# Kernel tuning notes

Measured on AMD Instinct MI355X. Metric: run time of the kernel, lower is better.

The kernel has to match this reference:

```python
import jax, jax.numpy as jnp
import numpy as np

B, T, D, H, C = 128, 1024, 3, 512, 3


def setup_inputs() -> dict:
    key = jax.random.key(0)
    ks = jax.random.split(key, 9)
    s = 1.0 / np.sqrt(H)
    u = lambda k, shp: jax.random.uniform(k, shp, jnp.float32, -s, s)
    return {
        'inputs': jax.random.normal(ks[0], (B, T, D), jnp.float32),
        'W': u(ks[1], (H, H)),
        'P': u(ks[2], (H, D)),
        'b_v': u(ks[3], (H, 1)),
        'W_z': u(ks[4], (H, H)),
        'P_z': u(ks[5], (H, D)),
        'b_z': u(ks[6], (H, 1)),
        'fc_W': u(ks[7], (C, H)),
        'fc_b': u(ks[8], (C,)),
    }


def reference(inputs, W, P, b_v, W_z, P_z, b_z, fc_W, fc_b):
    # Mask: second half of hidden units receive no direct input (rows H//2: of P zeroed)
    h = P.shape[0]
    P_m = jnp.concatenate([P[: h // 2], jnp.zeros_like(P[h // 2 :])], axis=0)
    bv = b_v[:, 0]
    bz = b_z[:, 0]

    def step(r, x_t):  # r: (B,H), x_t: (B,D)
        z = jax.nn.sigmoid(r @ W_z.T + x_t @ P_z.T + bz)
        cand = jax.nn.sigmoid(r @ W.T + x_t @ P_m.T + bv)
        r_new = (1.0 - z) * r + z * cand
        return r_new, r_new

    r0 = jnp.zeros((inputs.shape[0], h), inputs.dtype)
    xs = jnp.transpose(inputs, (1, 0, 2))  # (T,B,D)
    _, hs = jax.lax.scan(step, r0, xs)      # (T,B,H)
    hidden = jnp.transpose(hs, (1, 0, 2))   # (B,T,H)
    out = hidden @ fc_W.T + fc_b            # (B,T,C)
    return out, hidden
```

## Files before the change

### kernel.cpp

```cpp
#include <hip/hip_runtime.h>
#include <hip/hip_bf16.h>

#define BB 128
#define TT 1024
#define DD 3
#define HH 512
#define CC 3

#define NG 8
#define NCH 16
#define MB 16
#define HC 32

typedef __attribute__((ext_vector_type(8))) __bf16 bf16x8;
typedef __attribute__((ext_vector_type(4))) float f32x4;

__global__ __launch_bounds__(256, 1) void rnn_persist(
    const float* __restrict__ x,
    const float* __restrict__ W,
    const float* __restrict__ P,
    const float* __restrict__ bv,
    const float* __restrict__ Wz,
    const float* __restrict__ Pz,
    const float* __restrict__ bz,
    float* __restrict__ hidden,
    unsigned* __restrict__ Rbuf,
    unsigned* __restrict__ ready)
{
    __shared__ __align__(16) __bf16 Wl[64][520];
    __shared__ __align__(16) __bf16 Ra[16][520];
    __shared__ float pre[16][68];

    const int tid = threadIdx.x;
    const int bid = blockIdx.x;
    const int g   = bid & 7;
    const int ch  = bid >> 3;
    const int h0  = ch * HC;
    const int b0  = g * MB;

    for (int idx = tid; idx < 64 * 512; idx += 256) {
        int row = idx >> 9, col = idx & 511;
        float v = (row < 32) ? Wz[(h0 + row) * HH + col]
                             : W[(h0 + row - 32) * HH + col];
        Wl[row][col] = (__bf16)v;
    }

    const int lane = tid & 63;
    const int wv   = tid >> 6;
    const int frow = lane & 15;
    const int q    = lane >> 4;
    const int eb   = tid >> 4;
    const int ehp  = tid & 15;

    const int hl0 = 2 * ehp, hl1 = hl0 + 1;
    const int hg0 = h0 + hl0, hg1 = h0 + hl1;
    const float pzw00 = Pz[hg0*3+0], pzw01 = Pz[hg0*3+1], pzw02 = Pz[hg0*3+2];
    const float pzw10 = Pz[hg1*3+0], pzw11 = Pz[hg1*3+1], pzw12 = Pz[hg1*3+2];
    const float pvw00 = (hg0 < HH/2) ? P[hg0*3+0] : 0.f;
    const float pvw01 = (hg0 < HH/2) ? P[hg0*3+1] : 0.f;
    const float pvw02 = (hg0 < HH/2) ? P[hg0*3+2] : 0.f;
    const float pvw10 = (hg1 < HH/2) ? P[hg1*3+0] : 0.f;
    const float pvw11 = (hg1 < HH/2) ? P[hg1*3+1] : 0.f;
    const float pvw12 = (hg1 < HH/2) ? P[hg1*3+2] : 0.f;
    const float bzr0 = bz[hg0], bzr1 = bz[hg1];
    const float bvr0 = bv[hg0], bvr1 = bv[hg1];

    {
        uint2 cl; cl.x = 0xFFFFFFFFu; cl.y = 0xFFFFFFFFu;
        unsigned* d0 = Rbuf + (size_t)(b0 + eb) * HH + h0 + hl0;
        unsigned* d1 = d0 + BB * HH;
        asm volatile("global_store_dwordx2 %0, %2, off sc0 sc1\n\t"
                     "global_store_dwordx2 %1, %2, off sc0 sc1\n\t"
                     "s_waitcnt vmcnt(0)"
                     :: "v"(d0), "v"(d1), "v"(cl) : "memory");
    }
    __syncthreads();
    if (tid == 0)
        __hip_atomic_store(&ready[bid], 1u, __ATOMIC_RELAXED, __HIP_MEMORY_SCOPE_AGENT);
    if (tid < 16) {
        const unsigned* rp = &ready[tid * 8 + g];
        int spin = 0;
        while (__hip_atomic_load(rp, __ATOMIC_RELAXED, __HIP_MEMORY_SCOPE_AGENT) == 0u) {
            if (++spin > (1 << 20)) break;
        }
    }
    __syncthreads();

    bf16x8 Bfrag[16];
    #pragma unroll
    for (int ks = 0; ks < 16; ks++)
        Bfrag[ks] = *(const bf16x8*)&Wl[wv * 16 + frow][ks * 32 + q * 8];

    float rs0 = 0.f, rs1 = 0.f;
    const float* xptr = x + (size_t)(b0 + eb) * TT * DD;

    const int c4 = tid & 127;
    const int r0 = tid >> 7;
    char* rb = (char*)&Ra[0][0] + r0 * 1040 + c4 * 8;

    #define BAD4(G) ((((G).x ^ w16) | ((G).y ^ w16) | ((G).z ^ w16) | ((G).w ^ w16)) & 0xFFFFu)

    for (int t = 0; t < TT; t++) {
        float x0 = xptr[0], x1 = xptr[1], x2 = xptr[2];
        xptr += DD;

        float mz0, mz1, mc0, mc1;
        if (t > 0) {
            const unsigned w16 = (unsigned)t;
            const unsigned* bse = Rbuf + (size_t)(t & 1) * (BB * HH)
                                + (size_t)(b0 + r0) * HH + (c4 << 2);
            const uint4* q0 = (const uint4*)(bse);
            const uint4* q1 = (const uint4*)(bse + 1024);
            const uint4* q2 = (const uint4*)(bse + 2048);
            const uint4* q3 = (const uint4*)(bse + 3072);
            const uint4* q4 = (const uint4*)(bse + 4096);
            const uint4* q5 = (const uint4*)(bse + 5120);
            const uint4* q6 = (const uint4*)(bse + 6144);
            const uint4* q7 = (const uint4*)(bse + 7168);
            uint4 G0, G1, G2, G3, G4, G5, G6, G7;
            int spin = 0;
            for (;;) {
                asm volatile(
                    "global_load_dwordx4 %0, %8, off sc0 sc1\n\t"
                    "global_load_dwordx4 %1, %9, off sc0 sc1\n\t"
                    "global_load_dwordx4 %2, %10, off sc0 sc1\n\t"
                    "global_load_dwordx4 %3, %11, off sc0 sc1\n\t"
                    "global_load_dwordx4 %4, %12, off sc0 sc1\n\t"
                    "global_load_dwordx4 %5, %13, off sc0 sc1\n\t"
                    "global_load_dwordx4 %6, %14, off sc0 sc1\n\t"
                    "global_load_dwordx4 %7, %15, off sc0 sc1\n\t"
                    "s_waitcnt vmcnt(0)"
                    : "=&v"(G0), "=&v"(G1), "=&v"(G2), "=&v"(G3),
                      "=&v"(G4), "=&v"(G5), "=&v"(G6), "=&v"(G7)
                    : "v"(q0), "v"(q1), "v"(q2), "v"(q3),
                      "v"(q4), "v"(q5), "v"(q6), "v"(q7)
                    : "memory");
                unsigned bad = BAD4(G0) | BAD4(G1) | BAD4(G2) | BAD4(G3)
                             | BAD4(G4) | BAD4(G5) | BAD4(G6) | BAD4(G7);
                if (bad == 0u) break;
                if (++spin > (1 << 12)) break;
            }
            { uint2 o; o.x=(G0.x>>16)|(G0.y&0xFFFF0000u); o.y=(G0.z>>16)|(G0.w&0xFFFF0000u);
              *(uint2*)(rb + 0*2080) = o; }
            { uint2 o; o.x=(G1.x>>16)|(G1.y&0xFFFF0000u); o.y=(G1.z>>16)|(G1.w&0xFFFF0000u);
              *(uint2*)(rb + 1*2080) = o; }
            { uint2 o; o.x=(G2.x>>16)|(G2.y&0xFFFF0000u); o.y=(G2.z>>16)|(G2.w&0xFFFF0000u);
              *(uint2*)(rb + 2*2080) = o; }
            { uint2 o; o.x=(G3.x>>16)|(G3.y&0xFFFF0000u); o.y=(G3.z>>16)|(G3.w&0xFFFF0000u);
              *(uint2*)(rb + 3*2080) = o; }
            { uint2 o; o.x=(G4.x>>16)|(G4.y&0xFFFF0000u); o.y=(G4.z>>16)|(G4.w&0xFFFF0000u);
              *(uint2*)(rb + 4*2080) = o; }
            { uint2 o; o.x=(G5.x>>16)|(G5.y&0xFFFF0000u); o.y=(G5.z>>16)|(G5.w&0xFFFF0000u);
              *(uint2*)(rb + 5*2080) = o; }
            { uint2 o; o.x=(G6.x>>16)|(G6.y&0xFFFF0000u); o.y=(G6.z>>16)|(G6.w&0xFFFF0000u);
              *(uint2*)(rb + 6*2080) = o; }
            { uint2 o; o.x=(G7.x>>16)|(G7.y&0xFFFF0000u); o.y=(G7.z>>16)|(G7.w&0xFFFF0000u);
              *(uint2*)(rb + 7*2080) = o; }
            __syncthreads();

            f32x4 acc = {0.f, 0.f, 0.f, 0.f};
            #pragma unroll
            for (int ks = 0; ks < 16; ks++) {
                bf16x8 af = *(const bf16x8*)&Ra[frow][ks * 32 + q * 8];
                acc = __builtin_amdgcn_mfma_f32_16x16x32_bf16(af, Bfrag[ks], acc, 0, 0, 0);
            }
            #pragma unroll
            for (int r = 0; r < 4; r++)
                pre[q * 4 + r][wv * 16 + frow] = acc[r];
            __syncthreads();

            mz0 = pre[eb][hl0];      mz1 = pre[eb][hl1];
            mc0 = pre[eb][32 + hl0]; mc1 = pre[eb][32 + hl1];
        } else {
            mz0 = mz1 = mc0 = mc1 = 0.f;
        }

        float pz0 = mz0 + x0*pzw00 + x1*pzw01 + x2*pzw02 + bzr0;
        float pz1 = mz1 + x0*pzw10 + x1*pzw11 + x2*pzw12 + bzr1;
        float pv0 = mc0 + x0*pvw00 + x1*pvw01 + x2*pvw02 + bvr0;
        float pv1 = mc1 + x0*pvw10 + x1*pvw11 + x2*pvw12 + bvr1;
        float z0 = 1.f / (1.f + __expf(-pz0));
        float z1 = 1.f / (1.f + __expf(-pz1));
        float c0 = 1.f / (1.f + __expf(-pv0));
        float c1 = 1.f / (1.f + __expf(-pv1));
        rs0 = (1.f - z0) * rs0 + z0 * c0;
        rs1 = (1.f - z1) * rs1 + z1 * c1;

        if (t < TT - 1) {
            unsigned tagv = (unsigned)(t + 1);
            union { __bf16 h; unsigned short u; } a0, a1;
            a0.h = (__bf16)rs0; a1.h = (__bf16)rs1;
            uint2 d; d.x = ((unsigned)a0.u << 16) | tagv;
                     d.y = ((unsigned)a1.u << 16) | tagv;
            unsigned* dst = Rbuf + (size_t)((t + 1) & 1) * (BB * HH)
                          + (size_t)(b0 + eb) * HH + h0 + hl0;
            asm volatile("global_store_dwordx2 %0, %1, off sc0 sc1"
                         :: "v"(dst), "v"(d) : "memory");
        }
        union { float f[2]; uint2 u2; } hvu;
        hvu.f[0] = rs0; hvu.f[1] = rs1;
        float* hid = &hidden[((size_t)(b0 + eb) * TT + t) * HH + h0 + hl0];
        asm volatile("global_store_dwordx2 %0, %1, off"
                     :: "v"(hid), "v"(hvu.u2) : "memory");
    }
    #undef BAD4
}

__global__ __launch_bounds__(256) void fc_kernel(
    const float* __restrict__ hidden, const float* __restrict__ fcW,
    const float* __restrict__ fcb, float* __restrict__ out)
{
    const int lane = threadIdx.x & 63;
    const int wid  = (blockIdx.x * blockDim.x + threadIdx.x) >> 6;
    const int nw   = (gridDim.x * blockDim.x) >> 6;
    const int NR   = BB * TT;

    float w0[8], w1[8], w2[8];
    #pragma unroll
    for (int j = 0; j < 8; j++) {
        w0[j] = fcW[0 * HH + lane * 8 + j];
        w1[j] = fcW[1 * HH + lane * 8 + j];
        w2[j] = fcW[2 * HH + lane * 8 + j];
    }
    const float c0 = fcb[0], c1 = fcb[1], c2 = fcb[2];

    int row = wid;
    float4 va, vb;
    if (row < NR) {
        const float* hr = hidden + (size_t)row * HH + lane * 8;
        va = *(const float4*)hr;
        vb = *(const float4*)(hr + 4);
    }
    while (row < NR) {
        int nrow = row + nw;
        float4 na, nb;
        if (nrow < NR) {
            const float* hr = hidden + (size_t)nrow * HH + lane * 8;
            na = *(const float4*)hr;
            nb = *(const float4*)(hr + 4);
        }
        float s0 = va.x*w0[0] + va.y*w0[1] + va.z*w0[2] + va.w*w0[3]
                 + vb.x*w0[4] + vb.y*w0[5] + vb.z*w0[6] + vb.w*w0[7];
        float s1 = va.x*w1[0] + va.y*w1[1] + va.z*w1[2] + va.w*w1[3]
                 + vb.x*w1[4] + vb.y*w1[5] + vb.z*w1[6] + vb.w*w1[7];
        float s2 = va.x*w2[0] + va.y*w2[1] + va.z*w2[2] + va.w*w2[3]
                 + vb.x*w2[4] + vb.y*w2[5] + vb.z*w2[6] + vb.w*w2[7];
        #pragma unroll
        for (int off = 1; off < 64; off <<= 1) {
            s0 += __shfl_xor(s0, off);
            s1 += __shfl_xor(s1, off);
            s2 += __shfl_xor(s2, off);
        }
        if (lane == 0) {
            float* o = out + (size_t)row * CC;
            o[0] = s0 + c0; o[1] = s1 + c1; o[2] = s2 + c2;
        }
        row = nrow; va = na; vb = nb;
    }
}

extern "C" void kernel_launch(void* const* d_in, const int* in_sizes, int n_in,
                              void* d_out, int out_size, void* d_ws, size_t ws_size,
                              hipStream_t stream) {
    (void)in_sizes; (void)n_in; (void)out_size; (void)ws_size;
    const float* x   = (const float*)d_in[0];
    const float* W   = (const float*)d_in[1];
    const float* P   = (const float*)d_in[2];
    const float* bv  = (const float*)d_in[3];
    const float* Wz  = (const float*)d_in[4];
    const float* Pz  = (const float*)d_in[5];
    const float* bz  = (const float*)d_in[6];
    const float* fcW = (const float*)d_in[7];
    const float* fcb = (const float*)d_in[8];

    float* out    = (float*)d_out;
    float* hidden = out + (size_t)BB * TT * CC;

    unsigned* ready = (unsigned*)d_ws;
    unsigned* Rbuf  = (unsigned*)((char*)d_ws + 4096);

    hipMemsetAsync(d_ws, 0, 4096, stream);
    hipLaunchKernelGGL(rnn_persist, dim3(NG * NCH), dim3(256), 0, stream,
                       x, W, P, bv, Wz, Pz, bz, hidden, Rbuf, ready);
    hipLaunchKernelGGL(fc_kernel, dim3(1024), dim3(256), 0, stream,
                       hidden, fcW, fcb, out);
}
```

Measured before the change: 2.421 ms.

## Halve persistent blocks, widen hidden slice per block, add cheap tag pre-poll

Cuts the persistent RNN grid from 128 to 64 blocks, so each block owns 64 hidden units and runs two MFMA accumulators per wave against twice the LDS-resident weights. Each thread now handles four hidden units and writes 128-bit stores. Before the full-tile load, one wave polls a single tag word from each producer block and only then issues the bulk load. The aim is to reduce per-step cross-block synchronisation traffic and polling contention, at the cost of doubling per-block MFMA and elementwise work on the serial critical path.

```diff
diff --git a/kernel.cpp b/kernel.cpp
--- a/kernel.cpp
+++ b/kernel.cpp
@@ -8,12 +8,13 @@
 #define CC 3
 
 #define NG 8
-#define NCH 16
+#define NCH 8
 #define MB 16
-#define HC 32
+#define HC 64
 
 typedef __attribute__((ext_vector_type(8))) __bf16 bf16x8;
 typedef __attribute__((ext_vector_type(4))) float f32x4;
+typedef __attribute__((ext_vector_type(4))) unsigned u32x4;
 
 __global__ __launch_bounds__(256, 1) void rnn_persist(
     const float* __restrict__ x,
@@ -27,9 +28,9 @@
     unsigned* __restrict__ Rbuf,
     unsigned* __restrict__ ready)
 {
-    __shared__ __align__(16) __bf16 Wl[64][520];
+    __shared__ __align__(16) __bf16 Wl[128][520];
     __shared__ __align__(16) __bf16 Ra[16][520];
-    __shared__ float pre[16][68];
+    __shared__ float pre[16][132];
 
     const int tid = threadIdx.x;
     const int bid = blockIdx.x;
@@ -38,10 +39,10 @@
     const int h0  = ch * HC;
     const int b0  = g * MB;
 
-    for (int idx = tid; idx < 64 * 512; idx += 256) {
+    for (int idx = tid; idx < 128 * 512; idx += 256) {
         int row = idx >> 9, col = idx & 511;
-        float v = (row < 32) ? Wz[(h0 + row) * HH + col]
-                             : W[(h0 + row - 32) * HH + col];
+        float v = (row < 64) ? Wz[(h0 + row) * HH + col]
+                             : W[(h0 + row - 64) * HH + col];
         Wl[row][col] = (__bf16)v;
     }
 
@@ -50,48 +51,58 @@
     const int frow = lane & 15;
     const int q    = lane >> 4;
     const int eb   = tid >> 4;
-    const int ehp  = tid & 15;
-
-    const int hl0 = 2 * ehp, hl1 = hl0 + 1;
-    const int hg0 = h0 + hl0, hg1 = h0 + hl1;
-    const float pzw00 = Pz[hg0*3+0], pzw01 = Pz[hg0*3+1], pzw02 = Pz[hg0*3+2];
-    const float pzw10 = Pz[hg1*3+0], pzw11 = Pz[hg1*3+1], pzw12 = Pz[hg1*3+2];
-    const float pvw00 = (hg0 < HH/2) ? P[hg0*3+0] : 0.f;
-    const float pvw01 = (hg0 < HH/2) ? P[hg0*3+1] : 0.f;
-    const float pvw02 = (hg0 < HH/2) ? P[hg0*3+2] : 0.f;
-    const float pvw10 = (hg1 < HH/2) ? P[hg1*3+0] : 0.f;
-    const float pvw11 = (hg1 < HH/2) ? P[hg1*3+1] : 0.f;
-    const float pvw12 = (hg1 < HH/2) ? P[hg1*3+2] : 0.f;
-    const float bzr0 = bz[hg0], bzr1 = bz[hg1];
-    const float bvr0 = bv[hg0], bvr1 = bv[hg1];
+    const int ehq  = tid & 15;
+    const int hl   = ehq * 4;
+
+    const int hg0 = h0 + hl, hg1 = hg0 + 1, hg2 = hg0 + 2, hg3 = hg0 + 3;
+    const float pz00 = Pz[hg0*3+0], pz01 = Pz[hg0*3+1], pz02 = Pz[hg0*3+2];
+    const float pz10 = Pz[hg1*3+0], pz11 = Pz[hg1*3+1], pz12 = Pz[hg1*3+2];
+    const float pz20 = Pz[hg2*3+0], pz21 = Pz[hg2*3+1], pz22 = Pz[hg2*3+2];
+    const float pz30 = Pz[hg3*3+0], pz31 = Pz[hg3*3+1], pz32 = Pz[hg3*3+2];
+    const float pv00 = (hg0 < HH/2) ? P[hg0*3+0] : 0.f;
+    const float pv01 = (hg0 < HH/2) ? P[hg0*3+1] : 0.f;
+    const float pv02 = (hg0 < HH/2) ? P[hg0*3+2] : 0.f;
+    const float pv10 = (hg1 < HH/2) ? P[hg1*3+0] : 0.f;
+    const float pv11 = (hg1 < HH/2) ? P[hg1*3+1] : 0.f;
+    const float pv12 = (hg1 < HH/2) ? P[hg1*3+2] : 0.f;
+    const float pv20 = (hg2 < HH/2) ? P[hg2*3+0] : 0.f;
+    const float pv21 = (hg2 < HH/2) ? P[hg2*3+1] : 0.f;
+    const float pv22 = (hg2 < HH/2) ? P[hg2*3+2] : 0.f;
+    const float pv30 = (hg3 < HH/2) ? P[hg3*3+0] : 0.f;
+    const float pv31 = (hg3 < HH/2) ? P[hg3*3+1] : 0.f;
+    const float pv32 = (hg3 < HH/2) ? P[hg3*3+2] : 0.f;
+    const float bzr0 = bz[hg0], bzr1 = bz[hg1], bzr2 = bz[hg2], bzr3 = bz[hg3];
+    const float bvr0 = bv[hg0], bvr1 = bv[hg1], bvr2 = bv[hg2], bvr3 = bv[hg3];
 
     {
-        uint2 cl; cl.x = 0xFFFFFFFFu; cl.y = 0xFFFFFFFFu;
-        unsigned* d0 = Rbuf + (size_t)(b0 + eb) * HH + h0 + hl0;
+        u32x4 cl = {0xFFFFFFFFu, 0xFFFFFFFFu, 0xFFFFFFFFu, 0xFFFFFFFFu};
+        unsigned* d0 = Rbuf + (size_t)(b0 + eb) * HH + h0 + hl;
         unsigned* d1 = d0 + BB * HH;
-        asm volatile("global_store_dwordx2 %0, %2, off sc0 sc1\n\t"
-                     "global_store_dwordx2 %1, %2, off sc0 sc1\n\t"
+        asm volatile("global_store_dwordx4 %0, %2, off sc0 sc1\n\t"
+                     "global_store_dwordx4 %1, %2, off sc0 sc1\n\t"
                      "s_waitcnt vmcnt(0)"
                      :: "v"(d0), "v"(d1), "v"(cl) : "memory");
     }
     __syncthreads();
     if (tid == 0)
-        __hip_atomic_store(&ready[bid], 1u, __ATOMIC_RELAXED, __HIP_MEMORY_SCOPE_AGENT);
-    if (tid < 16) {
-        const unsigned* rp = &ready[tid * 8 + g];
+        __hip_atomic_store(&ready[g * 8 + ch], 1u, __ATOMIC_RELAXED, __HIP_MEMORY_SCOPE_AGENT);
+    if (tid < 8) {
+        const unsigned* rp = &ready[g * 8 + tid];
         int spin = 0;
         while (__hip_atomic_load(rp, __ATOMIC_RELAXED, __HIP_MEMORY_SCOPE_AGENT) == 0u) {
-            if (++spin > (1 << 20)) break;
+            if (++spin > (1 << 22)) break;
         }
     }
     __syncthreads();
 
-    bf16x8 Bfrag[16];
+    bf16x8 Bfrag0[16], Bfrag1[16];
     #pragma unroll
-    for (int ks = 0; ks < 16; ks++)
-        Bfrag[ks] = *(const bf16x8*)&Wl[wv * 16 + frow][ks * 32 + q * 8];
-
-    float rs0 = 0.f, rs1 = 0.f;
+    for (int ks = 0; ks < 16; ks++) {
+        Bfrag0[ks] = *(const bf16x8*)&Wl[wv * 32 +      frow][ks * 32 + q * 8];
+        Bfrag1[ks] = *(const bf16x8*)&Wl[wv * 32 + 16 + frow][ks * 32 + q * 8];
+    }
+
+    float rs0 = 0.f, rs1 = 0.f, rs2 = 0.f, rs3 = 0.f;
     const float* xptr = x + (size_t)(b0 + eb) * TT * DD;
 
     const int c4 = tid & 127;
@@ -104,20 +115,35 @@
         float x0 = xptr[0], x1 = xptr[1], x2 = xptr[2];
         xptr += DD;
 
-        float mz0, mz1, mc0, mc1;
+        float mz0, mz1, mz2, mz3, mc0, mc1, mc2, mc3;
         if (t > 0) {
             const unsigned w16 = (unsigned)t;
+            {
+                const unsigned* hp = Rbuf + (size_t)(t & 1) * (BB * HH)
+                                   + (size_t)b0 * HH + (lane & 7) * HC;
+                const bool act = (lane < 8);
+                int spin = 0;
+                for (;;) {
+                    unsigned v = w16;
+                    if (act)
+                        asm volatile("global_load_dword %0, %1, off sc0 sc1\n\t"
+                                     "s_waitcnt vmcnt(0)"
+                                     : "=&v"(v) : "v"(hp) : "memory");
+                    if (__all((int)((v & 0xFFFFu) == w16))) break;
+                    if (++spin > (1 << 14)) break;
+                }
+            }
             const unsigned* bse = Rbuf + (size_t)(t & 1) * (BB * HH)
                                 + (size_t)(b0 + r0) * HH + (c4 << 2);
-            const uint4* q0 = (const uint4*)(bse);
-            const uint4* q1 = (const uint4*)(bse + 1024);
-            const uint4* q2 = (const uint4*)(bse + 2048);
-            const uint4* q3 = (const uint4*)(bse + 3072);
-            const uint4* q4 = (const uint4*)(bse + 4096);
-            const uint4* q5 = (const uint4*)(bse + 5120);
-            const uint4* q6 = (const uint4*)(bse + 6144);
-            const uint4* q7 = (const uint4*)(bse + 7168);
-            uint4 G0, G1, G2, G3, G4, G5, G6, G7;
+            const unsigned* q0 = bse;
+            const unsigned* q1 = bse + 1024;
+            const unsigned* q2 = bse + 2048;
+            const unsigned* q3 = bse + 3072;
+            const unsigned* q4 = bse + 4096;
+            const unsigned* q5 = bse + 5120;
+            const unsigned* q6 = bse + 6144;
+            const unsigned* q7 = bse + 7168;
+            u32x4 G0, G1, G2, G3, G4, G5, G6, G7;
             int spin = 0;
             for (;;) {
                 asm volatile(
@@ -158,50 +184,69 @@
               *(uint2*)(rb + 7*2080) = o; }
             __syncthreads();
 
-            f32x4 acc = {0.f, 0.f, 0.f, 0.f};
+            f32x4 acc0 = {0.f, 0.f, 0.f, 0.f};
+            f32x4 acc1 = {0.f, 0.f, 0.f, 0.f};
             #pragma unroll
             for (int ks = 0; ks < 16; ks++) {
                 bf16x8 af = *(const bf16x8*)&Ra[frow][ks * 32 + q * 8];
-                acc = __builtin_amdgcn_mfma_f32_16x16x32_bf16(af, Bfrag[ks], acc, 0, 0, 0);
+                acc0 = __builtin_amdgcn_mfma_f32_16x16x32_bf16(af, Bfrag0[ks], acc0, 0, 0, 0);
+                acc1 = __builtin_amdgcn_mfma_f32_16x16x32_bf16(af, Bfrag1[ks], acc1, 0, 0, 0);
             }
             #pragma unroll
-            for (int r = 0; r < 4; r++)
-                pre[q * 4 + r][wv * 16 + frow] = acc[r];
+            for (int r = 0; r < 4; r++) {
+                pre[q * 4 + r][wv * 32 +      frow] = acc0[r];
+                pre[q * 4 + r][wv * 32 + 16 + frow] = acc1[r];
+            }
             __syncthreads();
 
-            mz0 = pre[eb][hl0];      mz1 = pre[eb][hl1];
-            mc0 = pre[eb][32 + hl0]; mc1 = pre[eb][32 + hl1];
+            mz0 = pre[eb][hl + 0];      mz1 = pre[eb][hl + 1];
+            mz2 = pre[eb][hl + 2];      mz3 = pre[eb][hl + 3];
+            mc0 = pre[eb][64 + hl + 0]; mc1 = pre[eb][64 + hl + 1];
+            mc2 = pre[eb][64 + hl + 2]; mc3 = pre[eb][64 + hl + 3];
         } else {
-            mz0 = mz1 = mc0 = mc1 = 0.f;
-        }
-
-        float pz0 = mz0 + x0*pzw00 + x1*pzw01 + x2*pzw02 + bzr0;
-        float pz1 = mz1 + x0*pzw10 + x1*pzw11 + x2*pzw12 + bzr1;
-        float pv0 = mc0 + x0*pvw00 + x1*pvw01 + x2*pvw02 + bvr0;
-        float pv1 = mc1 + x0*pvw10 + x1*pvw11 + x2*pvw12 + bvr1;
-        float z0 = 1.f / (1.f + __expf(-pz0));
-        float z1 = 1.f / (1.f + __expf(-pz1));
-        float c0 = 1.f / (1.f + __expf(-pv0));
-        float c1 = 1.f / (1.f + __expf(-pv1));
+            mz0 = mz1 = mz2 = mz3 = 0.f;
+            mc0 = mc1 = mc2 = mc3 = 0.f;
+        }
+
+        float pzq0 = mz0 + x0*pz00 + x1*pz01 + x2*pz02 + bzr0;
+        float pzq1 = mz1 + x0*pz10 + x1*pz11 + x2*pz12 + bzr1;
+        float pzq2 = mz2 + x0*pz20 + x1*pz21 + x2*pz22 + bzr2;
+        float pzq3 = mz3 + x0*pz30 + x1*pz31 + x2*pz32 + bzr3;
+        float pvq0 = mc0 + x0*pv00 + x1*pv01 + x2*pv02 + bvr0;
+        float pvq1 = mc1 + x0*pv10 + x1*pv11 + x2*pv12 + bvr1;
+        float pvq2 = mc2 + x0*pv20 + x1*pv21 + x2*pv22 + bvr2;
+        float pvq3 = mc3 + x0*pv30 + x1*pv31 + x2*pv32 + bvr3;
+        float z0 = 1.f / (1.f + __expf(-pzq0));
+        float z1 = 1.f / (1.f + __expf(-pzq1));
+        float z2 = 1.f / (1.f + __expf(-pzq2));
+        float z3 = 1.f / (1.f + __expf(-pzq3));
+        float c0 = 1.f / (1.f + __expf(-pvq0));
+        float c1 = 1.f / (1.f + __expf(-pvq1));
+        float c2 = 1.f / (1.f + __expf(-pvq2));
+        float c3 = 1.f / (1.f + __expf(-pvq3));
         rs0 = (1.f - z0) * rs0 + z0 * c0;
         rs1 = (1.f - z1) * rs1 + z1 * c1;
+        rs2 = (1.f - z2) * rs2 + z2 * c2;
+        rs3 = (1.f - z3) * rs3 + z3 * c3;
 
         if (t < TT - 1) {
             unsigned tagv = (unsigned)(t + 1);
-            union { __bf16 h; unsigned short u; } a0, a1;
+            union { __bf16 h; unsigned short u; } a0, a1, a2, a3;
             a0.h = (__bf16)rs0; a1.h = (__bf16)rs1;
-            uint2 d; d.x = ((unsigned)a0.u << 16) | tagv;
-                     d.y = ((unsigned)a1.u << 16) | tagv;
+            a2.h = (__bf16)rs2; a3.h = (__bf16)rs3;
+            u32x4 d = { ((unsigned)a0.u << 16) | tagv,
+                        ((unsigned)a1.u << 16) | tagv,
+                        ((unsigned)a2.u << 16) | tagv,
+                        ((unsigned)a3.u << 16) | tagv };
             unsigned* dst = Rbuf + (size_t)((t + 1) & 1) * (BB * HH)
-                          + (size_t)(b0 + eb) * HH + h0 + hl0;
-            asm volatile("global_store_dwordx2 %0, %1, off sc0 sc1"
+                          + (size_t)(b0 + eb) * HH + h0 + hl;
+            asm volatile("global_store_dwordx4 %0, %1, off sc0 sc1"
                          :: "v"(dst), "v"(d) : "memory");
         }
-        union { float f[2]; uint2 u2; } hvu;
-        hvu.f[0] = rs0; hvu.f[1] = rs1;
-        float* hid = &hidden[((size_t)(b0 + eb) * TT + t) * HH + h0 + hl0];
-        asm volatile("global_store_dwordx2 %0, %1, off"
-                     :: "v"(hid), "v"(hvu.u2) : "memory");
+        f32x4 hv = {rs0, rs1, rs2, rs3};
+        float* hid = &hidden[((size_t)(b0 + eb) * TT + t) * HH + h0 + hl];
+        asm volatile("global_store_dwordx4 %0, %1, off"
+                     :: "v"(hid), "v"(hv) : "memory");
     }
     #undef BAD4
 }
@@ -279,7 +324,7 @@
     unsigned* ready = (unsigned*)d_ws;
     unsigned* Rbuf  = (unsigned*)((char*)d_ws + 4096);
 
-    hipMemsetAsync(d_ws, 0, 4096, stream);
+    (void)hipMemsetAsync(d_ws, 0, 4096, stream);
     hipLaunchKernelGGL(rnn_persist, dim3(NG * NCH), dim3(256), 0, stream,
                        x, W, P, bv, Wz, Pz, bz, hidden, Rbuf, ready);
     hipLaunchKernelGGL(fc_kernel, dim3(1024), dim3(256), 0, stream,
```

New measurement: 2.673 ms. +10.4%, slower.
